# Optimization experiments

Hardware: AMD Instinct MI355X
Metric: run time of the kernel (lower is better)

## Reference

```python
import jax, jax.numpy as jnp
import numpy as np

B, D = 2048, 512

def setup_inputs() -> dict:
    key = jax.random.key(0)
    ks = jax.random.split(key, 9)
    s = 1.0 / np.sqrt(D)
    return {
        "query": jax.random.normal(ks[0], (B, D), jnp.float32),
        "key": jax.random.normal(ks[1], (B, D), jnp.float32),
        "value": jax.random.normal(ks[2], (B, D), jnp.float32),
        "Wq": jax.random.normal(ks[3], (D, D), jnp.float32) * s,
        "bq": jax.random.normal(ks[4], (D,), jnp.float32) * s,
        "Wk": jax.random.normal(ks[5], (D, D), jnp.float32) * s,
        "bk": jax.random.normal(ks[6], (D,), jnp.float32) * s,
        "Wv": jax.random.normal(ks[7], (D, D), jnp.float32) * s,
        "bv": jax.random.normal(ks[8], (D,), jnp.float32) * s,
    }

def reference(query, key, value, Wq, bq, Wk, bk, Wv, bv):
    # torch nn.Linear: y = x @ W.T + b
    q = query @ Wq.T + bq  # [B, D]
    k = key @ Wk.T + bk    # [B, D]
    v = value @ Wv.T + bv  # [B, D]
    # outer product per batch element: [B, D, 1] @ [B, 1, D] -> [B, D, D]
    attn = q[:, :, None] * k[:, None, :]
    score = jax.nn.softmax(attn, axis=-1)  # softmax over last D axis (no scaling, per source)
    # [B, D, D] @ [B, D, 1] -> [B, D, 1]
    out = jnp.einsum('bij,bj->bi', score, v)[:, :, None]
    return out
```

## Files before the change

kernel.cpp:

```cpp
#include <hip/hip_runtime.h>


#define B_SZ 2048
#define D_SZ 512
#define LOG2E 1.44269504088896340736f
#define NGRID 64
#define SEG 136

typedef __attribute__((ext_vector_type(2))) float  f32x2;
typedef __attribute__((ext_vector_type(4))) float  f32x4;
typedef __attribute__((ext_vector_type(8))) short  bf16x8;
typedef __attribute__((ext_vector_type(4))) unsigned short u16x4;
typedef __attribute__((ext_vector_type(8))) unsigned short u16x8;

__device__ __forceinline__ float exp2_raw(float x) {
#if defined(__has_builtin) && __has_builtin(__builtin_amdgcn_exp2f)
    return __builtin_amdgcn_exp2f(x);
#else
    return exp2f(x);
#endif
}

__device__ __forceinline__ f32x2 pk_fma(f32x2 a, f32x2 b, f32x2 c) {
    f32x2 d;
    asm("v_pk_fma_f32 %0, %1, %2, %3" : "=v"(d) : "v"(a), "v"(b), "v"(c));
    return d;
}
__device__ __forceinline__ f32x2 pk_add(f32x2 a, f32x2 b) {
    f32x2 d;
    asm("v_pk_add_f32 %0, %1, %2" : "=v"(d) : "v"(a), "v"(b));
    return d;
}
__device__ __forceinline__ f32x2 pk_mul(f32x2 a, f32x2 b) {
    f32x2 d;
    asm("v_pk_mul_f32 %0, %1, %2" : "=v"(d) : "v"(a), "v"(b));
    return d;
}

__device__ __forceinline__ void gload16(const void* g, void* l) {
    __builtin_amdgcn_global_load_lds(
        (const __attribute__((address_space(1))) unsigned int*)g,
        (__attribute__((address_space(3))) unsigned int*)l,
        16, 0, 0);
}

__device__ __forceinline__ void split1(float x, unsigned short& hi, unsigned short& lo) {
    unsigned int u = __float_as_uint(x);
    hi = (unsigned short)(u >> 16);
    float r = x - __uint_as_float(u & 0xFFFF0000u);
    lo = (unsigned short)(__float_as_uint(r) >> 16);
}

__device__ __forceinline__ void split4(const float4& x, u16x4& h, u16x4& l) {
    unsigned short hh, ll;
    split1(x.x, hh, ll); h.x = hh; l.x = ll;
    split1(x.y, hh, ll); h.y = hh; l.y = ll;
    split1(x.z, hh, ll); h.z = hh; l.z = ll;
    split1(x.w, hh, ll); h.w = hh; l.w = ll;
}

__global__ __launch_bounds__(256) void split_prepass(
    const float* __restrict__ Xq, const float* __restrict__ Xk, const float* __restrict__ Xv,
    const float* __restrict__ Wq, const float* __restrict__ Wk, const float* __restrict__ Wv,
    unsigned short* __restrict__ xhi, unsigned short* __restrict__ xlo,
    unsigned short* __restrict__ whi, unsigned short* __restrict__ wlo)
{
    const int z = blockIdx.z;
    const bool isW = (z >= 3);
    if (isW && blockIdx.x >= 128) return;

    const float* __restrict__ src =
        (z == 0) ? Xq : (z == 1) ? Xk : (z == 2) ? Xv :
        (z == 3) ? Wq : (z == 4) ? Wk : Wv;
    unsigned short* dh;
    unsigned short* dl;
    if (!isW) { size_t o = (size_t)z * B_SZ * D_SZ;       dh = xhi + o; dl = xlo + o; }
    else      { size_t o = (size_t)(z - 3) * D_SZ * D_SZ; dh = whi + o; dl = wlo + o; }

    const size_t i = ((size_t)blockIdx.x * 256 + threadIdx.x) * 8;
    const float s = (z == 4) ? LOG2E : 1.0f;

    float4 a = *(const float4*)(src + i);
    float4 b = *(const float4*)(src + i + 4);
    a.x *= s; a.y *= s; a.z *= s; a.w *= s;
    b.x *= s; b.y *= s; b.z *= s; b.w *= s;

    u16x4 h0, l0, h1, l1;
    split4(a, h0, l0);
    split4(b, h1, l1);
    u16x8 hh = {h0.x, h0.y, h0.z, h0.w, h1.x, h1.y, h1.z, h1.w};
    u16x8 ll = {l0.x, l0.y, l0.z, l0.w, l1.x, l1.y, l1.z, l1.w};
    *(u16x8*)(dh + i) = hh;
    *(u16x8*)(dl + i) = ll;
}

__global__ __launch_bounds__(256) void qkv_gemm_mfma(
    const unsigned short* __restrict__ xhi, const unsigned short* __restrict__ xlo,
    const unsigned short* __restrict__ whi, const unsigned short* __restrict__ wlo,
    const float* __restrict__ bq, const float* __restrict__ bk, const float* __restrict__ bv,
    float* __restrict__ qkv_out)
{
    const int which = blockIdx.z;
    const unsigned short* __restrict__ Ah = xhi + (size_t)which * B_SZ * D_SZ;
    const unsigned short* __restrict__ Al = xlo + (size_t)which * B_SZ * D_SZ;
    const unsigned short* __restrict__ Bh = whi + (size_t)which * D_SZ * D_SZ;
    const unsigned short* __restrict__ Bl = wlo + (size_t)which * D_SZ * D_SZ;
    const float* __restrict__ bias = (which == 0) ? bq : (which == 1) ? bk : bv;
    const float bscale = (which == 1) ? LOG2E : 1.0f;
    float* __restrict__ Y = qkv_out + (size_t)which * B_SZ * D_SZ;

    const int t    = threadIdx.x;
    const int lane = t & 63;
    const int wv   = t >> 6;
    const int l15  = lane & 15;
    const int quad = lane >> 4;
    const int wm   = (wv >> 1) * 32;
    const int wn   = (wv & 1) * 32;
    const int m0   = blockIdx.x * 64;
    const int n0   = blockIdx.y * 64;

    __shared__ unsigned short lds[2][4][64][32];

    f32x4 acc[2][2] = {};

    const unsigned short* __restrict__ gbase =
        (wv == 0) ? Ah : (wv == 1) ? Al : (wv == 2) ? Bh : Bl;
    const int tile0 = (wv < 2) ? m0 : n0;
    const size_t goff = (size_t)(tile0 + (lane >> 2)) * D_SZ + (lane & 3) * 8;

    auto stage = [&](int cur, int kk) {
        char* lb = (char*)&lds[cur][wv][0][0];
        const unsigned short* g = gbase + goff + kk;
#pragma unroll
        for (int h = 0; h < 4; ++h) {
            gload16(g + (size_t)h * 16 * D_SZ, lb + h * 1024);
        }
    };

    auto compute = [&](int cur) {
        bf16x8 a_h[2], a_l[2], b_h[2], b_l[2];
#pragma unroll
        for (int mi = 0; mi < 2; ++mi) {
            a_h[mi] = *(const bf16x8*)&lds[cur][0][wm + mi * 16 + l15][quad * 8];
            a_l[mi] = *(const bf16x8*)&lds[cur][1][wm + mi * 16 + l15][quad * 8];
        }
#pragma unroll
        for (int ni = 0; ni < 2; ++ni) {
            b_h[ni] = *(const bf16x8*)&lds[cur][2][wn + ni * 16 + l15][quad * 8];
            b_l[ni] = *(const bf16x8*)&lds[cur][3][wn + ni * 16 + l15][quad * 8];
        }
#pragma unroll
        for (int mi = 0; mi < 2; ++mi)
#pragma unroll
            for (int ni = 0; ni < 2; ++ni) {
                acc[mi][ni] = __builtin_amdgcn_mfma_f32_16x16x32_bf16(a_h[mi], b_h[ni], acc[mi][ni], 0, 0, 0);
                acc[mi][ni] = __builtin_amdgcn_mfma_f32_16x16x32_bf16(a_l[mi], b_h[ni], acc[mi][ni], 0, 0, 0);
                acc[mi][ni] = __builtin_amdgcn_mfma_f32_16x16x32_bf16(a_h[mi], b_l[ni], acc[mi][ni], 0, 0, 0);
            }
    };

    stage(0, 0);
    __syncthreads();
    int cur = 0;
    for (int it = 0; it < 15; ++it) {
        stage(cur ^ 1, (it + 1) * 32);
        compute(cur);
        __syncthreads();
        cur ^= 1;
    }
    compute(cur);

#pragma unroll
    for (int ni = 0; ni < 2; ++ni) {
        const int col = n0 + wn + ni * 16 + l15;
        const float bb = bias[col] * bscale;
#pragma unroll
        for (int mi = 0; mi < 2; ++mi) {
            const int row = m0 + wm + mi * 16 + quad * 4;
#pragma unroll
            for (int rr = 0; rr < 4; ++rr) {
                Y[(size_t)(row + rr) * D_SZ + col] = acc[mi][ni][rr] + bb;
            }
        }
    }
}

__global__ __launch_bounds__(256) void attn_kernel(
    const float* __restrict__ qkv, float* __restrict__ out)
{
    const int b = blockIdx.x;
    const int t = threadIdx.x;

    const float* __restrict__ q = qkv + (size_t)b * D_SZ;
    const float* __restrict__ k = qkv + (size_t)B_SZ * D_SZ + (size_t)b * D_SZ;
    const float* __restrict__ v = qkv + (size_t)2 * B_SZ * D_SZ + (size_t)b * D_SZ;

    __shared__ __align__(16) float kk_s[4 * SEG];
    __shared__ __align__(16) float vv_s[4 * SEG];
    __shared__ __align__(16) float fgrid[NGRID];
    __shared__ float redmax[4], redmin[4];

    const int i0 = t, i1 = t + 256;
    const float q0 = q[i0];
    const float q1 = q[i1];
    {
        const int j   = 2 * t;
        const int pos = (j >> 7) * SEG + (j & 127);
        float2 kf = *(const float2*)&k[j];
        float2 vf = *(const float2*)&v[j];
        *(float2*)&kk_s[pos] = kf;
        *(float2*)&vv_s[pos] = vf;
    }

    float qmax = fmaxf(q0, q1), qmin = fminf(q0, q1);
#pragma unroll
    for (int off = 32; off > 0; off >>= 1) {
        qmax = fmaxf(qmax, __shfl_xor(qmax, off));
        qmin = fminf(qmin, __shfl_xor(qmin, off));
    }
    const int wave = t >> 6;
    if ((t & 63) == 0) { redmax[wave] = qmax; redmin[wave] = qmin; }
    __syncthreads();
    qmax = fmaxf(fmaxf(redmax[0], redmax[1]), fmaxf(redmax[2], redmax[3]));
    qmin = fminf(fminf(redmin[0], redmin[1]), fminf(redmin[2], redmin[3]));

    const float h    = fmaxf((qmax - qmin) * (1.0f / (float)(NGRID - 3)), 1e-30f);
    const float s0   = qmin - h;
    const float invh = 1.0f / h;

    {
        const int   g   = t >> 2;
        const int   sub = t & 3;
        const int   jb  = sub * SEG;
        const float sg  = s0 + (float)g * h;
        const f32x2 sgg = {sg, sg};

        f32x2 dena = {0.f, 0.f}, denb = {0.f, 0.f};
        f32x2 numa = {0.f, 0.f}, numb = {0.f, 0.f};
#pragma unroll 4
        for (int jj = 0; jj < 128; jj += 4) {
            f32x4 kq = *(const f32x4*)&kk_s[jb + jj];
            f32x4 vq = *(const f32x4*)&vv_s[jb + jj];
            f32x2 ka = {kq.x, kq.y}, kb_ = {kq.z, kq.w};
            f32x2 va = {vq.x, vq.y}, vb_ = {vq.z, vq.w};

            f32x2 ea = pk_mul(sgg, ka);
            f32x2 eb = pk_mul(sgg, kb_);
            ea.x = exp2_raw(ea.x); ea.y = exp2_raw(ea.y);
            eb.x = exp2_raw(eb.x); eb.y = exp2_raw(eb.y);

            dena = pk_add(dena, ea);
            denb = pk_add(denb, eb);
            numa = pk_fma(ea, va, numa);
            numb = pk_fma(eb, vb_, numb);
        }
        float den = (dena.x + dena.y) + (denb.x + denb.y);
        float num = (numa.x + numa.y) + (numb.x + numb.y);
        den += __shfl_xor(den, 1);  num += __shfl_xor(num, 1);
        den += __shfl_xor(den, 2);  num += __shfl_xor(num, 2);
        if (sub == 0) fgrid[g] = num / den;
    }
    __syncthreads();

#pragma unroll
    for (int r = 0; r < 2; ++r) {
        const float qi = (r == 0) ? q0 : q1;
        const int   ii = (r == 0) ? i0 : i1;

        float u  = (qi - s0) * invh;
        int   ic = (int)floorf(u);
        ic = (ic < 1) ? 1 : ((ic > NGRID - 3) ? (NGRID - 3) : ic);
        float uu = u - (float)ic;

        float f0 = fgrid[ic - 1];
        float f1 = fgrid[ic];
        float f2 = fgrid[ic + 1];
        float f3 = fgrid[ic + 2];

        const float um1 = uu - 1.0f, um2 = uu - 2.0f, up1 = uu + 1.0f;
        const float w0 = -uu * um1 * um2 * (1.0f / 6.0f);
        const float w1 =  up1 * um1 * um2 * 0.5f;
        const float w2 = -up1 * uu  * um2 * 0.5f;
        const float w3 =  up1 * uu  * um1 * (1.0f / 6.0f);

        out[(size_t)b * D_SZ + ii] = w0 * f0 + w1 * f1 + w2 * f2 + w3 * f3;
    }
}

extern "C" void kernel_launch(void* const* d_in, const int* in_sizes, int n_in,
                              void* d_out, int out_size, void* d_ws, size_t ws_size,
                              hipStream_t stream) {
    const float* query = (const float*)d_in[0];
    const float* key_  = (const float*)d_in[1];
    const float* value = (const float*)d_in[2];
    const float* Wq    = (const float*)d_in[3];
    const float* bq    = (const float*)d_in[4];
    const float* Wk    = (const float*)d_in[5];
    const float* bk    = (const float*)d_in[6];
    const float* Wv    = (const float*)d_in[7];
    const float* bv    = (const float*)d_in[8];
    float* out = (float*)d_out;

    float* qkv = (float*)d_ws;
    unsigned short* xhi = (unsigned short*)(qkv + (size_t)3 * B_SZ * D_SZ);
    unsigned short* xlo = xhi + (size_t)3 * B_SZ * D_SZ;
    unsigned short* whi = xlo + (size_t)3 * B_SZ * D_SZ;
    unsigned short* wlo = whi + (size_t)3 * D_SZ * D_SZ;

    dim3 g0(512, 1, 6);
    split_prepass<<<g0, 256, 0, stream>>>(query, key_, value, Wq, Wk, Wv,
                                          xhi, xlo, whi, wlo);

    dim3 g1(B_SZ / 64, D_SZ / 64, 3);
    qkv_gemm_mfma<<<g1, 256, 0, stream>>>(xhi, xlo, whi, wlo, bq, bk, bv, qkv);

    attn_kernel<<<B_SZ, 256, 0, stream>>>(qkv, out);
}
```

Before: 109.0 us.

## Fuse bf16 hi/lo split into GEMM and drop the split prepass kernel

Removes the separate prepass that wrote bf16 hi/lo copies of the inputs and weights to workspace. The GEMM now loads fp32 tiles straight into LDS with an XOR-swizzled layout and does the hi/lo split in registers just before the MFMAs. The LOG2E scaling of k moves from the prepass and bias into the attention kernel's k load. This removes one launch and a full read-write pass over the inputs, but doubles the LDS bytes per tile and repeats the split ALU work for every tile reuse.

```diff
diff --git a/kernel.cpp b/kernel.cpp
--- a/kernel.cpp
+++ b/kernel.cpp
@@ -10,8 +10,6 @@
 typedef __attribute__((ext_vector_type(2))) float  f32x2;
 typedef __attribute__((ext_vector_type(4))) float  f32x4;
 typedef __attribute__((ext_vector_type(8))) short  bf16x8;
-typedef __attribute__((ext_vector_type(4))) unsigned short u16x4;
-typedef __attribute__((ext_vector_type(8))) unsigned short u16x8;
 
 __device__ __forceinline__ float exp2_raw(float x) {
 #if defined(__has_builtin) && __has_builtin(__builtin_amdgcn_exp2f)
@@ -51,62 +49,29 @@
     lo = (unsigned short)(__float_as_uint(r) >> 16);
 }
 
-__device__ __forceinline__ void split4(const float4& x, u16x4& h, u16x4& l) {
+__device__ __forceinline__ void split8(const f32x4 p0, const f32x4 p1,
+                                       bf16x8& h, bf16x8& l) {
     unsigned short hh, ll;
-    split1(x.x, hh, ll); h.x = hh; l.x = ll;
-    split1(x.y, hh, ll); h.y = hh; l.y = ll;
-    split1(x.z, hh, ll); h.z = hh; l.z = ll;
-    split1(x.w, hh, ll); h.w = hh; l.w = ll;
-}
-
-__global__ __launch_bounds__(256) void split_prepass(
+    split1(p0.x, hh, ll); h[0] = (short)hh; l[0] = (short)ll;
+    split1(p0.y, hh, ll); h[1] = (short)hh; l[1] = (short)ll;
+    split1(p0.z, hh, ll); h[2] = (short)hh; l[2] = (short)ll;
+    split1(p0.w, hh, ll); h[3] = (short)hh; l[3] = (short)ll;
+    split1(p1.x, hh, ll); h[4] = (short)hh; l[4] = (short)ll;
+    split1(p1.y, hh, ll); h[5] = (short)hh; l[5] = (short)ll;
+    split1(p1.z, hh, ll); h[6] = (short)hh; l[6] = (short)ll;
+    split1(p1.w, hh, ll); h[7] = (short)hh; l[7] = (short)ll;
+}
+
+__global__ __launch_bounds__(256) void qkv_gemm_mfma(
     const float* __restrict__ Xq, const float* __restrict__ Xk, const float* __restrict__ Xv,
     const float* __restrict__ Wq, const float* __restrict__ Wk, const float* __restrict__ Wv,
-    unsigned short* __restrict__ xhi, unsigned short* __restrict__ xlo,
-    unsigned short* __restrict__ whi, unsigned short* __restrict__ wlo)
-{
-    const int z = blockIdx.z;
-    const bool isW = (z >= 3);
-    if (isW && blockIdx.x >= 128) return;
-
-    const float* __restrict__ src =
-        (z == 0) ? Xq : (z == 1) ? Xk : (z == 2) ? Xv :
-        (z == 3) ? Wq : (z == 4) ? Wk : Wv;
-    unsigned short* dh;
-    unsigned short* dl;
-    if (!isW) { size_t o = (size_t)z * B_SZ * D_SZ;       dh = xhi + o; dl = xlo + o; }
-    else      { size_t o = (size_t)(z - 3) * D_SZ * D_SZ; dh = whi + o; dl = wlo + o; }
-
-    const size_t i = ((size_t)blockIdx.x * 256 + threadIdx.x) * 8;
-    const float s = (z == 4) ? LOG2E : 1.0f;
-
-    float4 a = *(const float4*)(src + i);
-    float4 b = *(const float4*)(src + i + 4);
-    a.x *= s; a.y *= s; a.z *= s; a.w *= s;
-    b.x *= s; b.y *= s; b.z *= s; b.w *= s;
-
-    u16x4 h0, l0, h1, l1;
-    split4(a, h0, l0);
-    split4(b, h1, l1);
-    u16x8 hh = {h0.x, h0.y, h0.z, h0.w, h1.x, h1.y, h1.z, h1.w};
-    u16x8 ll = {l0.x, l0.y, l0.z, l0.w, l1.x, l1.y, l1.z, l1.w};
-    *(u16x8*)(dh + i) = hh;
-    *(u16x8*)(dl + i) = ll;
-}
-
-__global__ __launch_bounds__(256) void qkv_gemm_mfma(
-    const unsigned short* __restrict__ xhi, const unsigned short* __restrict__ xlo,
-    const unsigned short* __restrict__ whi, const unsigned short* __restrict__ wlo,
     const float* __restrict__ bq, const float* __restrict__ bk, const float* __restrict__ bv,
     float* __restrict__ qkv_out)
 {
     const int which = blockIdx.z;
-    const unsigned short* __restrict__ Ah = xhi + (size_t)which * B_SZ * D_SZ;
-    const unsigned short* __restrict__ Al = xlo + (size_t)which * B_SZ * D_SZ;
-    const unsigned short* __restrict__ Bh = whi + (size_t)which * D_SZ * D_SZ;
-    const unsigned short* __restrict__ Bl = wlo + (size_t)which * D_SZ * D_SZ;
+    const float* __restrict__ X    = (which == 0) ? Xq : (which == 1) ? Xk : Xv;
+    const float* __restrict__ W    = (which == 0) ? Wq : (which == 1) ? Wk : Wv;
     const float* __restrict__ bias = (which == 0) ? bq : (which == 1) ? bk : bv;
-    const float bscale = (which == 1) ? LOG2E : 1.0f;
     float* __restrict__ Y = qkv_out + (size_t)which * B_SZ * D_SZ;
 
     const int t    = threadIdx.x;
@@ -119,35 +84,45 @@
     const int m0   = blockIdx.x * 64;
     const int n0   = blockIdx.y * 64;
 
-    __shared__ unsigned short lds[2][4][64][32];
+    __shared__ float lds[2][2][64][32];
 
     f32x4 acc[2][2] = {};
 
-    const unsigned short* __restrict__ gbase =
-        (wv == 0) ? Ah : (wv == 1) ? Al : (wv == 2) ? Bh : Bl;
-    const int tile0 = (wv < 2) ? m0 : n0;
-    const size_t goff = (size_t)(tile0 + (lane >> 2)) * D_SZ + (lane & 3) * 8;
+    const int   op    = wv >> 1;
+    const int   wsub  = wv & 1;
+    const float* __restrict__ gsrc = (op == 0) ? X : W;
+    const int   tile0 = (op == 0) ? m0 : n0;
+    const int grow   = tile0 + wsub * 32 + (lane >> 3);
+    const int gcolsw = ((lane & 7) ^ ((lane >> 3) & 7)) * 4;
+    const float* gl0 = gsrc + (size_t)grow * D_SZ + gcolsw;
 
     auto stage = [&](int cur, int kk) {
-        char* lb = (char*)&lds[cur][wv][0][0];
-        const unsigned short* g = gbase + goff + kk;
+        char* lb = (char*)&lds[cur][op][wsub * 32][0];
+        const float* g = gl0 + kk;
 #pragma unroll
         for (int h = 0; h < 4; ++h) {
-            gload16(g + (size_t)h * 16 * D_SZ, lb + h * 1024);
+            gload16(g + (size_t)(h * 8) * D_SZ, lb + h * 1024);
         }
     };
 
     auto compute = [&](int cur) {
         bf16x8 a_h[2], a_l[2], b_h[2], b_l[2];
+        const int sw = l15 & 7;
+        const int g0 = (quad << 1) ^ sw;
+        const int g1 = ((quad << 1) | 1) ^ sw;
 #pragma unroll
         for (int mi = 0; mi < 2; ++mi) {
-            a_h[mi] = *(const bf16x8*)&lds[cur][0][wm + mi * 16 + l15][quad * 8];
-            a_l[mi] = *(const bf16x8*)&lds[cur][1][wm + mi * 16 + l15][quad * 8];
+            const float* rp = &lds[cur][0][wm + mi * 16 + l15][0];
+            f32x4 p0 = *(const f32x4*)(rp + (g0 << 2));
+            f32x4 p1 = *(const f32x4*)(rp + (g1 << 2));
+            split8(p0, p1, a_h[mi], a_l[mi]);
         }
 #pragma unroll
         for (int ni = 0; ni < 2; ++ni) {
-            b_h[ni] = *(const bf16x8*)&lds[cur][2][wn + ni * 16 + l15][quad * 8];
-            b_l[ni] = *(const bf16x8*)&lds[cur][3][wn + ni * 16 + l15][quad * 8];
+            const float* rp = &lds[cur][1][wn + ni * 16 + l15][0];
+            f32x4 p0 = *(const f32x4*)(rp + (g0 << 2));
+            f32x4 p1 = *(const f32x4*)(rp + (g1 << 2));
+            split8(p0, p1, b_h[ni], b_l[ni]);
         }
 #pragma unroll
         for (int mi = 0; mi < 2; ++mi)
@@ -173,7 +148,7 @@
 #pragma unroll
     for (int ni = 0; ni < 2; ++ni) {
         const int col = n0 + wn + ni * 16 + l15;
-        const float bb = bias[col] * bscale;
+        const float bb = bias[col];
 #pragma unroll
         for (int mi = 0; mi < 2; ++mi) {
             const int row = m0 + wm + mi * 16 + quad * 4;
@@ -208,6 +183,8 @@
         const int pos = (j >> 7) * SEG + (j & 127);
         float2 kf = *(const float2*)&k[j];
         float2 vf = *(const float2*)&v[j];
+        kf.x *= LOG2E;
+        kf.y *= LOG2E;
         *(float2*)&kk_s[pos] = kf;
         *(float2*)&vv_s[pos] = vf;
     }
@@ -302,17 +279,10 @@
     float* out = (float*)d_out;
 
     float* qkv = (float*)d_ws;
-    unsigned short* xhi = (unsigned short*)(qkv + (size_t)3 * B_SZ * D_SZ);
-    unsigned short* xlo = xhi + (size_t)3 * B_SZ * D_SZ;
-    unsigned short* whi = xlo + (size_t)3 * B_SZ * D_SZ;
-    unsigned short* wlo = whi + (size_t)3 * D_SZ * D_SZ;
-
-    dim3 g0(512, 1, 6);
-    split_prepass<<<g0, 256, 0, stream>>>(query, key_, value, Wq, Wk, Wv,
-                                          xhi, xlo, whi, wlo);
 
     dim3 g1(B_SZ / 64, D_SZ / 64, 3);
-    qkv_gemm_mfma<<<g1, 256, 0, stream>>>(xhi, xlo, whi, wlo, bq, bk, bv, qkv);
+    qkv_gemm_mfma<<<g1, 256, 0, stream>>>(query, key_, value, Wq, Wk, Wv,
+                                          bq, bk, bv, qkv);
 
     attn_kernel<<<B_SZ, 256, 0, stream>>>(qkv, out);
 }
```

New measurement: 105.2 us. 1.04x faster.
